# Performance work log

Hardware: AMD Instinct MI355X
Metric: run time of the kernel (lower is better)

The kernel has to match this reference:

```python
import jax, jax.numpy as jnp
import numpy as np

B, S, D, H, KV, HD = 2, 2048, 1024, 16, 4, 64
NUM_BUCKETS, MAX_DIST = 32, 128


def _rel_pos_bucket(rel_pos, num_buckets=NUM_BUCKETS, max_distance=MAX_DIST):
    # bidirectional (is_decoder=False) T5 bucketing
    nb = num_buckets // 2
    buckets = (rel_pos > 0).astype(jnp.int32) * nb
    rel = jnp.abs(rel_pos)
    max_exact = nb // 2
    is_small = rel < max_exact
    rel_f = jnp.maximum(rel, 1).astype(jnp.float32)
    large = max_exact + (
        jnp.log(rel_f / max_exact) / np.log(max_distance / max_exact) * (nb - max_exact)
    ).astype(jnp.int32)
    large = jnp.minimum(large, nb - 1)
    return buckets + jnp.where(is_small, rel, large)


def _pool_weight(W, scale, apply_scale):
    # W: [inner_dim, d_model] (torch Linear layout). Optionally scale per head,
    # group-sum heads into kv_heads, broadcast back to n_heads.
    Wh = W.reshape(H, HD, D)                       # [H, hd, D]
    if apply_scale:
        # torch path: W.T -> [D,H,hd] * scale[H,1] -> back; equivalent per-head scale
        Wh = Wh * scale[:, :, None]                # scale: [H,1] -> [H,1,1]
    Wg = Wh.reshape(KV, H // KV, HD, D).sum(axis=1)  # [KV, hd, D]
    Wb = jnp.repeat(Wg, H // KV, axis=0)           # [H, hd, D]
    return Wb.reshape(H * HD, D)


def setup_inputs() -> dict:
    key = jax.random.key(0)
    ks = jax.random.split(key, 8)
    s = 1.0 / np.sqrt(D)
    return {
        "hidden_states": jax.random.normal(ks[0], (B, S, D), jnp.float32),
        "Wq": jax.random.normal(ks[1], (H * HD, D), jnp.float32) * s,
        "Wk": jax.random.normal(ks[2], (H * HD, D), jnp.float32) * s,
        "Wv": jax.random.normal(ks[3], (H * HD, D), jnp.float32) * s,
        "Wo": jax.random.normal(ks[4], (D, H * HD), jnp.float32) * s,
        "key_scale": jax.random.normal(ks[5], (H, 1), jnp.float32),
        "value_scale": jax.random.normal(ks[6], (H, 1), jnp.float32),
        "bias_emb": jax.random.normal(ks[7], (NUM_BUCKETS, H), jnp.float32),
    }


def reference(hidden_states, Wq, Wk, Wv, Wo, key_scale, value_scale, bias_emb):
    x = hidden_states
    # Q projection -> [B, H, S, hd]
    q = (x @ Wq.T).reshape(B, S, H, HD).transpose(0, 2, 1, 3)

    # K weight: per-head scale applied, then pooled. V weight: the original code
    # computes the scaled version but then (bug, replicated faithfully) pools the
    # RAW v weight, so value_scale has no effect on the forward math.
    Wk_eff = _pool_weight(Wk, key_scale, apply_scale=True)
    Wv_eff = _pool_weight(Wv, value_scale, apply_scale=False)

    k = (x @ Wk_eff.T).reshape(B, S, H, HD).transpose(0, 2, 1, 3)
    v = (x @ Wv_eff.T).reshape(B, S, H, HD).transpose(0, 2, 1, 3)

    # T5 attention: no 1/sqrt(d) scaling
    scores = jnp.einsum("bhqd,bhkd->bhqk", q, k)  # [B,H,S,S]

    # relative position bias
    ctx = jnp.arange(S)[:, None]
    mem = jnp.arange(S)[None, :]
    buckets = _rel_pos_bucket(mem - ctx)            # [S, S]
    pos_bias = bias_emb[buckets]                    # [S, S, H]
    pos_bias = pos_bias.transpose(2, 0, 1)[None]    # [1, H, S, S]

    scores = scores + pos_bias
    attn = jax.nn.softmax(scores.astype(jnp.float32), axis=-1).astype(scores.dtype)
    out = jnp.einsum("bhqk,bhkd->bhqd", attn, v)    # [B,H,S,hd]
    out = out.transpose(0, 2, 1, 3).reshape(B, S, H * HD)
    return out @ Wo.T                               # [B, S, D]
```

## Files before the change

kernel.cpp:

```cpp
#include <hip/hip_runtime.h>

using half8  = __attribute__((ext_vector_type(8))) _Float16;
using half4  = __attribute__((ext_vector_type(4))) _Float16;
using half2v = __attribute__((ext_vector_type(2))) _Float16;
using fp16x2 = __attribute__((ext_vector_type(2))) __fp16;
using f32x4  = __attribute__((ext_vector_type(4))) float;

#define BB 2
#define SS 2048
#define DD 1024
#define HH 16
#define KVH 4
#define HDIM 64
#define NQK 1280
#define LOG2E 1.4426950408889634f

#define GLDS(g, l) __builtin_amdgcn_global_load_lds( \
    (const __attribute__((address_space(1))) void*)(g), \
    (__attribute__((address_space(3))) void*)(l), 16, 0, 0)

__device__ __forceinline__ f32x4 mfma16(half4 a, half4 b, f32x4 c) {
    return __builtin_amdgcn_mfma_f32_16x16x16f16(a, b, c, 0, 0, 0);
}

__device__ __forceinline__ float fexp2(float x) {
#if __has_builtin(__builtin_amdgcn_exp2f)
    return __builtin_amdgcn_exp2f(x);
#else
    return exp2f(x);
#endif
}

__device__ __forceinline__ half2v cvt_pk_f16(float a, float b) {
    fp16x2 r = __builtin_amdgcn_cvt_pkrtz(a, b);
    return __builtin_bit_cast(half2v, r);
}

__device__ __forceinline__ int kv_off(int row, int hcol) {
    return row * 64 + ((((hcol >> 3) ^ row) & 7) << 3) + (hcol & 7);
}

__device__ __forceinline__ int gm_off(int row, int slot) {
    return row * 32 + (((slot ^ row) & 3) << 3);
}

__device__ __forceinline__ int rel_large(int rel) {
    int n;
    if (rel < 12) n = 0; else if (rel < 16) n = 1; else if (rel < 23) n = 2;
    else if (rel < 32) n = 3; else if (rel < 46) n = 4; else if (rel < 64) n = 5;
    else if (rel < 91) n = 6; else if (rel < 128) n = 7; else n = 8;
    int large = 8 + n;
    return large > 15 ? 15 : large;
}

__global__ void prep_all(const float* __restrict__ x,
                         const float* __restrict__ Wq, const float* __restrict__ Wk,
                         const float* __restrict__ Wv, const float* __restrict__ Wo,
                         const float* __restrict__ ksc, const float* __restrict__ bias_emb,
                         _Float16* __restrict__ Wqk, _Float16* __restrict__ Wvb,
                         _Float16* __restrict__ Wob, float* __restrict__ tab,
                         _Float16* __restrict__ Xh)
{
    int bid = blockIdx.x;
    if (bid < 2560) {
        int row = bid;
        int c = threadIdx.x * 4;
        if (row < NQK) {
            if (row < 1024) {
                #pragma unroll
                for (int j = 0; j < 4; ++j)
                    Wqk[(size_t)row * DD + c + j] = (_Float16)(Wq[(size_t)row * DD + c + j] * LOG2E);
            } else {
                int kh = row - 1024;
                int kvi = kh >> 6, hd = kh & 63;
                #pragma unroll
                for (int j = 0; j < 4; ++j) {
                    float s = 0.f;
                    #pragma unroll
                    for (int g = 0; g < 4; ++g)
                        s += Wk[(size_t)((kvi * 4 + g) * 64 + hd) * DD + c + j] * ksc[kvi * 4 + g];
                    Wqk[(size_t)row * DD + c + j] = (_Float16)s;
                }
            }
        } else if (row < 1536) {
            int vh = row - 1280;
            int kvi = vh >> 6, hd = vh & 63;
            #pragma unroll
            for (int j = 0; j < 4; ++j) {
                float s = 0.f;
                #pragma unroll
                for (int g = 0; g < 4; ++g)
                    s += Wv[(size_t)((kvi * 4 + g) * 64 + hd) * DD + c + j];
                Wvb[(size_t)vh * DD + c + j] = (_Float16)s;
            }
        } else {
            int r = row - 1536;
            #pragma unroll
            for (int j = 0; j < 4; ++j)
                Wob[(size_t)r * DD + c + j] = (_Float16)Wo[(size_t)r * DD + c + j];
        }
    } else if (bid < 6656) {
        int idx = ((bid - 2560) * 256 + threadIdx.x) * 4;
        float4 v = *(const float4*)(x + idx);
        half4 o = { (_Float16)v.x, (_Float16)v.y, (_Float16)v.z, (_Float16)v.w };
        *(half4*)(Xh + idx) = o;
    } else {
        int idx = (bid - 6656) * 256 + threadIdx.x;
        if (idx < HH * 4095) {
            int h = idx / 4095;
            int dpos = idx % 4095;
            int d = dpos - 2047;
            int rel = d < 0 ? -d : d;
            int bucket = (rel < 8) ? rel : rel_large(rel);
            if (d > 0) bucket += 16;
            tab[(size_t)h * 4095 + dpos] = bias_emb[bucket * HH + h] * LOG2E;
        }
    }
}

template<int OUTK>
__global__ __launch_bounds__(256) void gemm_bt(const _Float16* __restrict__ A,
                                               const _Float16* __restrict__ B,
                                               void* __restrict__ C0,
                                               _Float16* __restrict__ C1,
                                               int M, int K, int ldc)
{
    __shared__ __align__(16) _Float16 As[2][128 * 32];
    __shared__ __align__(16) _Float16 Bs[2][128 * 32];

    int nwg = gridDim.x * gridDim.y;
    int lid = blockIdx.y * gridDim.x + blockIdx.x;
    int sid = (lid & 7) * (nwg >> 3) + (lid >> 3);
    int m0 = (sid / gridDim.x) * 128, n0 = (sid % gridDim.x) * 128;

    int t = threadIdx.x;
    int wv = t >> 6, lane = t & 63;
    int wm = wv >> 1, wn = wv & 1;
    int lr = lane & 15, lg = lane >> 4;
    int srow = lane >> 2;
    int scol = (((lane & 3) ^ ((lane >> 2) & 3)) << 3);
    f32x4 acc[4][4] = {};

#define GSTAGE(BUF, K0)                                                       \
    {                                                                         \
        _Pragma("unroll")                                                     \
        for (int i_ = 0; i_ < 2; ++i_) {                                      \
            int chunk_ = wv * 2 + i_;                                         \
            int row_ = chunk_ * 16 + srow;                                    \
            GLDS(A + (size_t)(m0 + row_) * K + (K0) + scol,                   \
                 &As[BUF][chunk_ * 512 + lane * 8]);                          \
            GLDS(B + (size_t)(n0 + row_) * K + (K0) + scol,                   \
                 &Bs[BUF][chunk_ * 512 + lane * 8]);                          \
        }                                                                     \
    }

    GSTAGE(0, 0);
    __syncthreads();
    int cur = 0;

    for (int k0 = 0; k0 < K; k0 += 32) {
        if (k0 + 32 < K) GSTAGE(cur ^ 1, k0 + 32);
        half8 af[4], bfr[4];
        #pragma unroll
        for (int mi = 0; mi < 4; ++mi)
            af[mi] = *(const half8*)(&As[cur][gm_off(wm * 64 + mi * 16 + lr, lg)]);
        #pragma unroll
        for (int ni = 0; ni < 4; ++ni)
            bfr[ni] = *(const half8*)(&Bs[cur][gm_off(wn * 64 + ni * 16 + lr, lg)]);
        __builtin_amdgcn_s_setprio(1);
        #pragma unroll
        for (int mi = 0; mi < 4; ++mi)
            #pragma unroll
            for (int ni = 0; ni < 4; ++ni)
                acc[mi][ni] = __builtin_amdgcn_mfma_f32_16x16x32_f16(af[mi], bfr[ni], acc[mi][ni], 0, 0, 0);
        __builtin_amdgcn_s_setprio(0);
        __syncthreads();
        cur ^= 1;
    }
#undef GSTAGE

    #pragma unroll
    for (int mi = 0; mi < 4; ++mi) {
        #pragma unroll
        for (int ni = 0; ni < 4; ++ni) {
            int rowb = m0 + wm * 64 + mi * 16 + 4 * lg;
            int col  = n0 + wn * 64 + ni * 16 + lr;
            if constexpr (OUTK == 0) {
                #pragma unroll
                for (int r = 0; r < 4; ++r)
                    ((float*)C0)[(size_t)(rowb + r) * ldc + col] = acc[mi][ni][r];
            } else {
                if (n0 < 1280) {
                    #pragma unroll
                    for (int r = 0; r < 4; ++r)
                        ((_Float16*)C0)[(size_t)(rowb + r) * ldc + col] = (_Float16)acc[mi][ni][r];
                } else {
                    half4 o = { (_Float16)acc[mi][ni][0], (_Float16)acc[mi][ni][1],
                                (_Float16)acc[mi][ni][2], (_Float16)acc[mi][ni][3] };
                    *(half4*)(C1 + (size_t)(col - 1280) * M + rowb) = o;
                }
            }
        }
    }
}

__global__ __launch_bounds__(256) void attn(const _Float16* __restrict__ Y,
                                            const _Float16* __restrict__ Vt,
                                            const float* __restrict__ tab,
                                            _Float16* __restrict__ O)
{
    int blk = (blockIdx.x & 7) * 128 + (blockIdx.x >> 3);
    int qb = blk & 31, h = (blk >> 5) & 15, b = blk >> 9;
    int kv = h >> 2;
    int q0 = qb * 64;
    int t = threadIdx.x, w = t >> 6, lane = t & 63, lr = lane & 15, lg = lane >> 4;

    __shared__ __align__(16) _Float16 Ks[2][64 * 64];
    __shared__ __align__(16) _Float16 Vst[2][64 * 64];
    __shared__ float bias_s[2][128];

    const size_t yoff = (size_t)(b * SS + q0 + w * 16 + lr) * NQK + h * 64;
    half8 aq0 = *(const half8*)(Y + yoff + lg * 8);
    half8 aq1 = *(const half8*)(Y + yoff + 32 + lg * 8);

    const float bias_neg = tab[(size_t)h * 4095 + 0];
    const float bias_pos = tab[(size_t)h * 4095 + 4094];

    f32x4 acc_o[4] = {};
    float m = -1e30f, l = 0.f;
    const int bb = 63 - w * 16 - lr + 4 * lg;

    uint4 kreg0, kreg1, vreg0, vreg1;
    float breg = 0.f;
    const int srow = t >> 3, sc8 = (t & 7) << 3;
    const int srow1 = srow + 32;

#define ATTN_LOAD(KEY0)                                                          \
    {                                                                            \
        int k0_ = (KEY0);                                                        \
        kreg0 = *(const uint4*)(Y + (size_t)(b * SS + k0_ + srow)  * NQK + 1024 + kv * 64 + sc8); \
        kreg1 = *(const uint4*)(Y + (size_t)(b * SS + k0_ + srow1) * NQK + 1024 + kv * 64 + sc8); \
        vreg0 = *(const uint4*)(Vt + (size_t)(kv * 64 + srow)  * 4096 + b * SS + k0_ + sc8); \
        vreg1 = *(const uint4*)(Vt + (size_t)(kv * 64 + srow1) * 4096 + b * SS + k0_ + sc8); \
        bool far_ = (k0_ >= q0 + 192) || (k0_ <= q0 - 192);                      \
        if (!far_ && t < 128) {                                                  \
            int ti = k0_ - q0 + t - 63 + 2047;                                   \
            ti = ti < 0 ? 0 : (ti > 4094 ? 4094 : ti);                           \
            breg = tab[(size_t)h * 4095 + ti];                                   \
        }                                                                        \
    }

#define ATTN_WRITE(BUF, KEY0)                                                    \
    {                                                                            \
        int bf_ = (BUF);                                                         \
        *(uint4*)(&Ks[bf_][kv_off(srow,  sc8)]) = kreg0;                         \
        *(uint4*)(&Ks[bf_][kv_off(srow1, sc8)]) = kreg1;                         \
        *(uint4*)(&Vst[bf_][kv_off(srow,  sc8)]) = vreg0;                        \
        *(uint4*)(&Vst[bf_][kv_off(srow1, sc8)]) = vreg1;                        \
        bool far_ = ((KEY0) >= q0 + 192) || ((KEY0) <= q0 - 192);                \
        if (!far_ && t < 128) bias_s[bf_][t] = breg;                             \
    }

    ATTN_LOAD(0);
    ATTN_WRITE(0, 0);
    __syncthreads();
    int cur = 0;

    for (int key0 = 0; key0 < SS; key0 += 64) {
        if (key0 + 64 < SS) ATTN_LOAD(key0 + 64);

        const _Float16* ks = Ks[cur];
        const _Float16* vs = Vst[cur];
        bool far = (key0 >= q0 + 192) || (key0 <= q0 - 192);

        f32x4 z = {0.f, 0.f, 0.f, 0.f};
        f32x4 sc[4];
        __builtin_amdgcn_s_setprio(1);
        #pragma unroll
        for (int dt = 0; dt < 4; ++dt) {
            half8 bk0 = *(const half8*)(&ks[kv_off(dt * 16 + lr, lg * 8)]);
            half8 bk1 = *(const half8*)(&ks[kv_off(dt * 16 + lr, 32 + lg * 8)]);
            sc[dt] = __builtin_amdgcn_mfma_f32_16x16x32_f16(bk0, aq0, z, 0, 0, 0);
            sc[dt] = __builtin_amdgcn_mfma_f32_16x16x32_f16(bk1, aq1, sc[dt], 0, 0, 0);
        }
        __builtin_amdgcn_s_setprio(0);

        float c;
        if (!far) {
            #pragma unroll
            for (int dt = 0; dt < 4; ++dt)
                #pragma unroll
                for (int r = 0; r < 4; ++r)
                    sc[dt][r] += bias_s[cur][bb + dt * 16 + r];
            c = 0.f;
        } else {
            c = (key0 > q0) ? bias_pos : bias_neg;
        }

        float pmax = sc[0][0];
        #pragma unroll
        for (int dt = 0; dt < 4; ++dt)
            #pragma unroll
            for (int r = 0; r < 4; ++r) pmax = fmaxf(pmax, sc[dt][r]);
        pmax = fmaxf(pmax, __shfl_xor(pmax, 16, 64));
        pmax = fmaxf(pmax, __shfl_xor(pmax, 32, 64));
        pmax += c;
        if (__any(pmax > m + 8.f)) {
            float mn = fmaxf(m, pmax);
            float scale = fexp2(m - mn);
            l *= scale;
            #pragma unroll
            for (int odt = 0; odt < 4; ++odt)
                #pragma unroll
                for (int r = 0; r < 4; ++r) acc_o[odt][r] *= scale;
            m = mn;
        }
        float moff = m - c;
        float rs = 0.f;
        #pragma unroll
        for (int dt = 0; dt < 4; ++dt)
            #pragma unroll
            for (int r = 0; r < 4; ++r) {
                float p = fexp2(sc[dt][r] - moff);
                sc[dt][r] = p;
                rs += p;
            }
        rs += __shfl_xor(rs, 16, 64);
        rs += __shfl_xor(rs, 32, 64);
        l += rs;

        half4 pf[4];
        #pragma unroll
        for (int dt = 0; dt < 4; ++dt) {
            half2v p01 = cvt_pk_f16(sc[dt][0], sc[dt][1]);
            half2v p23 = cvt_pk_f16(sc[dt][2], sc[dt][3]);
            pf[dt] = { p01[0], p01[1], p23[0], p23[1] };
        }

        __builtin_amdgcn_s_setprio(1);
        #pragma unroll
        for (int odt = 0; odt < 4; ++odt)
            #pragma unroll
            for (int dt = 0; dt < 4; ++dt) {
                half4 vf = *(const half4*)(&vs[kv_off(odt * 16 + lr, dt * 16 + 4 * lg)]);
                acc_o[odt] = mfma16(vf, pf[dt], acc_o[odt]);
            }
        __builtin_amdgcn_s_setprio(0);

        if (key0 + 64 < SS) {
            ATTN_WRITE(cur ^ 1, key0 + 64);
            __syncthreads();
            cur ^= 1;
        }
    }

    float inv = 1.f / l;
    _Float16* orow = O + (size_t)(b * SS + q0 + w * 16 + lr) * 1024 + h * 64;
    #pragma unroll
    for (int odt = 0; odt < 4; ++odt) {
        half4 o = { (_Float16)(acc_o[odt][0] * inv), (_Float16)(acc_o[odt][1] * inv),
                    (_Float16)(acc_o[odt][2] * inv), (_Float16)(acc_o[odt][3] * inv) };
        *(half4*)(orow + odt * 16 + 4 * lg) = o;
    }
#undef ATTN_LOAD
#undef ATTN_WRITE
}

extern "C" void kernel_launch(void* const* d_in, const int* in_sizes, int n_in,
                              void* d_out, int out_size, void* d_ws, size_t ws_size,
                              hipStream_t stream)
{
    const float* x   = (const float*)d_in[0];
    const float* Wq  = (const float*)d_in[1];
    const float* Wk  = (const float*)d_in[2];
    const float* Wv  = (const float*)d_in[3];
    const float* Wo  = (const float*)d_in[4];
    const float* ksc = (const float*)d_in[5];
    const float* bias_emb = (const float*)d_in[7];
    float* out = (float*)d_out;

    char* ws = (char*)d_ws;
    _Float16* Wqk = (_Float16*)(ws);
    _Float16* Wvb = (_Float16*)(ws + 2621440);
    _Float16* Wob = (_Float16*)(ws + 3145728);
    float*    tab = (float*)(ws + 5242880);
    _Float16* Xh  = (_Float16*)(ws + 5505024);
    _Float16* Y   = (_Float16*)(ws + 13893632);
    _Float16* Vt  = (_Float16*)(ws + 24379392);
    _Float16* Ob  = (_Float16*)(ws + 26476544);

    prep_all<<<6912, 256, 0, stream>>>(x, Wq, Wk, Wv, Wo, ksc, bias_emb,
                                       Wqk, Wvb, Wob, tab, Xh);

    gemm_bt<3><<<dim3(12, 32), 256, 0, stream>>>(Xh, Wqk, Y, Vt, 4096, 1024, NQK);

    attn<<<1024, 256, 0, stream>>>(Y, Vt, tab, Ob);

    gemm_bt<0><<<dim3(8, 32), 256, 0, stream>>>(Ob, Wob, out, nullptr, 4096, 1024, 1024);
}
```

Before: 131.6 us.

## Fuse fp32-to-fp16 conversion into GEMM loads and enlarge attention query tiles

The separate prep passes that converted x and Wo to fp16 are removed. The GEMMs now load the fp32 operand through registers, convert it, and write it into LDS, while the other fp16 operand still uses direct global-to-LDS loads. This drops an extra round trip through memory for the activations and output weights, but it adds register pressure and VGPR-staged loads inside the GEMM main loop. Separately, the attention kernel is widened to 512 threads handling 128 queries per block, so each K/V tile in LDS is reused across twice as many queries, with the bias window and far-tile test adjusted to match.

```diff
diff --git a/kernel.cpp b/kernel.cpp
--- a/kernel.cpp
+++ b/kernel.cpp
@@ -36,6 +36,11 @@
     return __builtin_bit_cast(half2v, r);
 }
 
+__device__ __forceinline__ half8 cvt8_rte(float4 a, float4 b) {
+    return half8{ (_Float16)a.x, (_Float16)a.y, (_Float16)a.z, (_Float16)a.w,
+                  (_Float16)b.x, (_Float16)b.y, (_Float16)b.z, (_Float16)b.w };
+}
+
 __device__ __forceinline__ int kv_off(int row, int hcol) {
     return row * 64 + ((((hcol >> 3) ^ row) & 7) << 3) + (hcol & 7);
 }
@@ -53,59 +58,46 @@
     return large > 15 ? 15 : large;
 }
 
-__global__ void prep_all(const float* __restrict__ x,
-                         const float* __restrict__ Wq, const float* __restrict__ Wk,
-                         const float* __restrict__ Wv, const float* __restrict__ Wo,
-                         const float* __restrict__ ksc, const float* __restrict__ bias_emb,
+__global__ void prep_all(const float* __restrict__ Wq, const float* __restrict__ Wk,
+                         const float* __restrict__ Wv, const float* __restrict__ ksc,
+                         const float* __restrict__ bias_emb,
                          _Float16* __restrict__ Wqk, _Float16* __restrict__ Wvb,
-                         _Float16* __restrict__ Wob, float* __restrict__ tab,
-                         _Float16* __restrict__ Xh)
+                         float* __restrict__ tab)
 {
     int bid = blockIdx.x;
-    if (bid < 2560) {
+    if (bid < NQK) {
         int row = bid;
         int c = threadIdx.x * 4;
-        if (row < NQK) {
-            if (row < 1024) {
-                #pragma unroll
-                for (int j = 0; j < 4; ++j)
-                    Wqk[(size_t)row * DD + c + j] = (_Float16)(Wq[(size_t)row * DD + c + j] * LOG2E);
-            } else {
-                int kh = row - 1024;
-                int kvi = kh >> 6, hd = kh & 63;
-                #pragma unroll
-                for (int j = 0; j < 4; ++j) {
-                    float s = 0.f;
-                    #pragma unroll
-                    for (int g = 0; g < 4; ++g)
-                        s += Wk[(size_t)((kvi * 4 + g) * 64 + hd) * DD + c + j] * ksc[kvi * 4 + g];
-                    Wqk[(size_t)row * DD + c + j] = (_Float16)s;
-                }
-            }
-        } else if (row < 1536) {
-            int vh = row - 1280;
-            int kvi = vh >> 6, hd = vh & 63;
+        if (row < 1024) {
+            #pragma unroll
+            for (int j = 0; j < 4; ++j)
+                Wqk[(size_t)row * DD + c + j] = (_Float16)(Wq[(size_t)row * DD + c + j] * LOG2E);
+        } else {
+            int kh = row - 1024;
+            int kvi = kh >> 6, hd = kh & 63;
             #pragma unroll
             for (int j = 0; j < 4; ++j) {
                 float s = 0.f;
                 #pragma unroll
                 for (int g = 0; g < 4; ++g)
-                    s += Wv[(size_t)((kvi * 4 + g) * 64 + hd) * DD + c + j];
-                Wvb[(size_t)vh * DD + c + j] = (_Float16)s;
+                    s += Wk[(size_t)((kvi * 4 + g) * 64 + hd) * DD + c + j] * ksc[kvi * 4 + g];
+                Wqk[(size_t)row * DD + c + j] = (_Float16)s;
             }
-        } else {
-            int r = row - 1536;
-            #pragma unroll
-            for (int j = 0; j < 4; ++j)
-                Wob[(size_t)r * DD + c + j] = (_Float16)Wo[(size_t)r * DD + c + j];
-        }
-    } else if (bid < 6656) {
-        int idx = ((bid - 2560) * 256 + threadIdx.x) * 4;
-        float4 v = *(const float4*)(x + idx);
-        half4 o = { (_Float16)v.x, (_Float16)v.y, (_Float16)v.z, (_Float16)v.w };
-        *(half4*)(Xh + idx) = o;
+        }
+    } else if (bid < 1536) {
+        int vh = bid - 1280;
+        int kvi = vh >> 6, hd = vh & 63;
+        int c = threadIdx.x * 4;
+        #pragma unroll
+        for (int j = 0; j < 4; ++j) {
+            float s = 0.f;
+            #pragma unroll
+            for (int g = 0; g < 4; ++g)
+                s += Wv[(size_t)((kvi * 4 + g) * 64 + hd) * DD + c + j];
+            Wvb[(size_t)vh * DD + c + j] = (_Float16)s;
+        }
     } else {
-        int idx = (bid - 6656) * 256 + threadIdx.x;
+        int idx = (bid - 1536) * 256 + threadIdx.x;
         if (idx < HH * 4095) {
             int h = idx / 4095;
             int dpos = idx % 4095;
@@ -118,9 +110,9 @@
     }
 }
 
-template<int OUTK>
-__global__ __launch_bounds__(256) void gemm_bt(const _Float16* __restrict__ A,
-                                               const _Float16* __restrict__ B,
+template<int MODE>
+__global__ __launch_bounds__(256) void gemm_bt(const void* __restrict__ Ap,
+                                               const void* __restrict__ Bp,
                                                void* __restrict__ C0,
                                                _Float16* __restrict__ C1,
                                                int M, int K, int ldc)
@@ -138,28 +130,72 @@
     int wm = wv >> 1, wn = wv & 1;
     int lr = lane & 15, lg = lane >> 4;
     int srow = lane >> 2;
-    int scol = (((lane & 3) ^ ((lane >> 2) & 3)) << 3);
+    int scol = (((lane & 3) ^ (srow & 3)) << 3);
+    int fcol = (lane & 3) << 3;
     f32x4 acc[4][4] = {};
-
-#define GSTAGE(BUF, K0)                                                       \
+    float4 xr[2][2];
+
+    const _Float16* Ah = (const _Float16*)Ap;
+    const float*    Af = (const float*)Ap;
+    const _Float16* Bh = (const _Float16*)Bp;
+    const float*    Bf = (const float*)Bp;
+
+#define FLOAD_PH(K0)                                                          \
+    {                                                                         \
+        _Pragma("unroll")                                                     \
+        for (int i_ = 0; i_ < 2; ++i_) {                                      \
+            int row_ = (wv * 2 + i_) * 16 + srow;                             \
+            if constexpr (MODE == 1) {                                        \
+                const float* p_ = Af + (size_t)(m0 + row_) * K + (K0) + fcol; \
+                xr[i_][0] = *(const float4*)p_;                               \
+                xr[i_][1] = *(const float4*)(p_ + 4);                         \
+            } else {                                                          \
+                const float* p_ = Bf + (size_t)(n0 + row_) * K + (K0) + fcol; \
+                xr[i_][0] = *(const float4*)p_;                               \
+                xr[i_][1] = *(const float4*)(p_ + 4);                         \
+            }                                                                 \
+        }                                                                     \
+    }
+
+#define GLDS_PH(BUF, K0)                                                      \
     {                                                                         \
         _Pragma("unroll")                                                     \
         for (int i_ = 0; i_ < 2; ++i_) {                                      \
             int chunk_ = wv * 2 + i_;                                         \
             int row_ = chunk_ * 16 + srow;                                    \
-            GLDS(A + (size_t)(m0 + row_) * K + (K0) + scol,                   \
-                 &As[BUF][chunk_ * 512 + lane * 8]);                          \
-            GLDS(B + (size_t)(n0 + row_) * K + (K0) + scol,                   \
-                 &Bs[BUF][chunk_ * 512 + lane * 8]);                          \
+            if constexpr (MODE == 1)                                          \
+                GLDS(Bh + (size_t)(n0 + row_) * K + (K0) + scol,              \
+                     &Bs[BUF][chunk_ * 512 + lane * 8]);                      \
+            else                                                              \
+                GLDS(Ah + (size_t)(m0 + row_) * K + (K0) + scol,              \
+                     &As[BUF][chunk_ * 512 + lane * 8]);                      \
         }                                                                     \
     }
 
-    GSTAGE(0, 0);
+#define WRITE_PH(BUF)                                                         \
+    {                                                                         \
+        _Pragma("unroll")                                                     \
+        for (int i_ = 0; i_ < 2; ++i_) {                                      \
+            int chunk_ = wv * 2 + i_;                                         \
+            int off_ = chunk_ * 512 + srow * 32 + (((lane & 3) ^ (srow & 3)) << 3); \
+            half8 hv_ = cvt8_rte(xr[i_][0], xr[i_][1]);                       \
+            if constexpr (MODE == 1) *(half8*)(&As[BUF][off_]) = hv_;         \
+            else                     *(half8*)(&Bs[BUF][off_]) = hv_;         \
+        }                                                                     \
+    }
+
+    FLOAD_PH(0);
+    GLDS_PH(0, 0);
+    WRITE_PH(0);
     __syncthreads();
     int cur = 0;
 
     for (int k0 = 0; k0 < K; k0 += 32) {
-        if (k0 + 32 < K) GSTAGE(cur ^ 1, k0 + 32);
+        bool more = (k0 + 32 < K);
+        if (more) {
+            FLOAD_PH(k0 + 32);
+            GLDS_PH(cur ^ 1, k0 + 32);
+        }
         half8 af[4], bfr[4];
         #pragma unroll
         for (int mi = 0; mi < 4; ++mi)
@@ -174,10 +210,13 @@
             for (int ni = 0; ni < 4; ++ni)
                 acc[mi][ni] = __builtin_amdgcn_mfma_f32_16x16x32_f16(af[mi], bfr[ni], acc[mi][ni], 0, 0, 0);
         __builtin_amdgcn_s_setprio(0);
+        if (more) WRITE_PH(cur ^ 1);
         __syncthreads();
         cur ^= 1;
     }
-#undef GSTAGE
+#undef FLOAD_PH
+#undef GLDS_PH
+#undef WRITE_PH
 
     #pragma unroll
     for (int mi = 0; mi < 4; ++mi) {
@@ -185,7 +224,7 @@
         for (int ni = 0; ni < 4; ++ni) {
             int rowb = m0 + wm * 64 + mi * 16 + 4 * lg;
             int col  = n0 + wn * 64 + ni * 16 + lr;
-            if constexpr (OUTK == 0) {
+            if constexpr (MODE == 0) {
                 #pragma unroll
                 for (int r = 0; r < 4; ++r)
                     ((float*)C0)[(size_t)(rowb + r) * ldc + col] = acc[mi][ni][r];
@@ -204,20 +243,20 @@
     }
 }
 
-__global__ __launch_bounds__(256) void attn(const _Float16* __restrict__ Y,
+__global__ __launch_bounds__(512) void attn(const _Float16* __restrict__ Y,
                                             const _Float16* __restrict__ Vt,
                                             const float* __restrict__ tab,
                                             _Float16* __restrict__ O)
 {
-    int blk = (blockIdx.x & 7) * 128 + (blockIdx.x >> 3);
-    int qb = blk & 31, h = (blk >> 5) & 15, b = blk >> 9;
+    int blk = (blockIdx.x & 7) * 64 + (blockIdx.x >> 3);
+    int qb = blk & 15, h = (blk >> 4) & 15, b = blk >> 8;
     int kv = h >> 2;
-    int q0 = qb * 64;
+    int q0 = qb * 128;
     int t = threadIdx.x, w = t >> 6, lane = t & 63, lr = lane & 15, lg = lane >> 4;
 
     __shared__ __align__(16) _Float16 Ks[2][64 * 64];
     __shared__ __align__(16) _Float16 Vst[2][64 * 64];
-    __shared__ float bias_s[2][128];
+    __shared__ float bias_s[2][192];
 
     const size_t yoff = (size_t)(b * SS + q0 + w * 16 + lr) * NQK + h * 64;
     half8 aq0 = *(const half8*)(Y + yoff + lg * 8);
@@ -228,23 +267,21 @@
 
     f32x4 acc_o[4] = {};
     float m = -1e30f, l = 0.f;
-    const int bb = 63 - w * 16 - lr + 4 * lg;
-
-    uint4 kreg0, kreg1, vreg0, vreg1;
+    const int bb = 127 - w * 16 - lr + 4 * lg;
+
+    uint4 kreg, vreg;
     float breg = 0.f;
     const int srow = t >> 3, sc8 = (t & 7) << 3;
-    const int srow1 = srow + 32;
+
+#define FAR(K0) (((K0) >= q0 + 256) || ((K0) <= q0 - 192))
 
 #define ATTN_LOAD(KEY0)                                                          \
     {                                                                            \
         int k0_ = (KEY0);                                                        \
-        kreg0 = *(const uint4*)(Y + (size_t)(b * SS + k0_ + srow)  * NQK + 1024 + kv * 64 + sc8); \
-        kreg1 = *(const uint4*)(Y + (size_t)(b * SS + k0_ + srow1) * NQK + 1024 + kv * 64 + sc8); \
-        vreg0 = *(const uint4*)(Vt + (size_t)(kv * 64 + srow)  * 4096 + b * SS + k0_ + sc8); \
-        vreg1 = *(const uint4*)(Vt + (size_t)(kv * 64 + srow1) * 4096 + b * SS + k0_ + sc8); \
-        bool far_ = (k0_ >= q0 + 192) || (k0_ <= q0 - 192);                      \
-        if (!far_ && t < 128) {                                                  \
-            int ti = k0_ - q0 + t - 63 + 2047;                                   \
+        kreg = *(const uint4*)(Y + (size_t)(b * SS + k0_ + srow) * NQK + 1024 + kv * 64 + sc8); \
+        vreg = *(const uint4*)(Vt + (size_t)(kv * 64 + srow) * 4096 + b * SS + k0_ + sc8); \
+        if (!FAR(k0_) && t < 192) {                                              \
+            int ti = k0_ - q0 + t + 1920;                                        \
             ti = ti < 0 ? 0 : (ti > 4094 ? 4094 : ti);                           \
             breg = tab[(size_t)h * 4095 + ti];                                   \
         }                                                                        \
@@ -253,12 +290,9 @@
 #define ATTN_WRITE(BUF, KEY0)                                                    \
     {                                                                            \
         int bf_ = (BUF);                                                         \
-        *(uint4*)(&Ks[bf_][kv_off(srow,  sc8)]) = kreg0;                         \
-        *(uint4*)(&Ks[bf_][kv_off(srow1, sc8)]) = kreg1;                         \
-        *(uint4*)(&Vst[bf_][kv_off(srow,  sc8)]) = vreg0;                        \
-        *(uint4*)(&Vst[bf_][kv_off(srow1, sc8)]) = vreg1;                        \
-        bool far_ = ((KEY0) >= q0 + 192) || ((KEY0) <= q0 - 192);                \
-        if (!far_ && t < 128) bias_s[bf_][t] = breg;                             \
+        *(uint4*)(&Ks[bf_][kv_off(srow, sc8)]) = kreg;                           \
+        *(uint4*)(&Vst[bf_][kv_off(srow, sc8)]) = vreg;                          \
+        if (!FAR(KEY0) && t < 192) bias_s[bf_][t] = breg;                        \
     }
 
     ATTN_LOAD(0);
@@ -271,7 +305,7 @@
 
         const _Float16* ks = Ks[cur];
         const _Float16* vs = Vst[cur];
-        bool far = (key0 >= q0 + 192) || (key0 <= q0 - 192);
+        bool far = FAR(key0);
 
         f32x4 z = {0.f, 0.f, 0.f, 0.f};
         f32x4 sc[4];
@@ -364,6 +398,7 @@
     }
 #undef ATTN_LOAD
 #undef ATTN_WRITE
+#undef FAR
 }
 
 extern "C" void kernel_launch(void* const* d_in, const int* in_sizes, int n_in,
@@ -382,19 +417,16 @@
     char* ws = (char*)d_ws;
     _Float16* Wqk = (_Float16*)(ws);
     _Float16* Wvb = (_Float16*)(ws + 2621440);
-    _Float16* Wob = (_Float16*)(ws + 3145728);
-    float*    tab = (float*)(ws + 5242880);
-    _Float16* Xh  = (_Float16*)(ws + 5505024);
-    _Float16* Y   = (_Float16*)(ws + 13893632);
-    _Float16* Vt  = (_Float16*)(ws + 24379392);
-    _Float16* Ob  = (_Float16*)(ws + 26476544);
-
-    prep_all<<<6912, 256, 0, stream>>>(x, Wq, Wk, Wv, Wo, ksc, bias_emb,
-                                       Wqk, Wvb, Wob, tab, Xh);
-
-    gemm_bt<3><<<dim3(12, 32), 256, 0, stream>>>(Xh, Wqk, Y, Vt, 4096, 1024, NQK);
-
-    attn<<<1024, 256, 0, stream>>>(Y, Vt, tab, Ob);
-
-    gemm_bt<0><<<dim3(8, 32), 256, 0, stream>>>(Ob, Wob, out, nullptr, 4096, 1024, 1024);
-}
+    float*    tab = (float*)(ws + 3145728);
+    _Float16* Y   = (_Float16*)(ws + 3407872);
+    _Float16* Vt  = (_Float16*)(ws + 13893632);
+    _Float16* Ob  = (_Float16*)(ws + 15990784);
+
+    prep_all<<<1792, 256, 0, stream>>>(Wq, Wk, Wv, ksc, bias_emb, Wqk, Wvb, tab);
+
+    gemm_bt<1><<<dim3(12, 32), 256, 0, stream>>>(x, Wqk, Y, Vt, 4096, 1024, NQK);
+
+    attn<<<512, 512, 0, stream>>>(Y, Vt, tab, Ob);
+
+    gemm_bt<0><<<dim3(8, 32), 256, 0, stream>>>(Ob, Wo, out, nullptr, 4096, 1024, 1024);
+}
```

Result: no change. 132.4 us (+0.6%).
